# Kernel tuning notes

Measured on AMD Instinct MI355X. Metric: run time of the kernel, lower is better.

Reference implementation:

```python
import jax, jax.numpy as jnp
import numpy as np

TEMPERATURE = 0.5


def _cos_sim_flat(a, b):
    # row-normalize then full similarity matrix, flattened (matches torch.mm(a_n, b_n.T).flatten())
    a_n = a / jnp.linalg.norm(a, axis=1, keepdims=True)
    b_n = b / jnp.linalg.norm(b, axis=1, keepdims=True)
    return (a_n @ b_n.T).reshape(-1)


def setup_inputs() -> dict:
    key = jax.random.key(0)
    k1, k2, k3 = jax.random.split(key, 3)
    N, D = 4096, 2048
    return {
        "x_source": jax.random.normal(k1, (N, D), dtype=jnp.float32),
        "x_bc_target": jax.random.normal(k2, (N, D), dtype=jnp.float32),
        "x_raw_target": jax.random.normal(k3, (N, D), dtype=jnp.float32),
    }


def reference(x_source, x_bc_target, x_raw_target):
    sim_pos = _cos_sim_flat(x_source, x_bc_target)  # [N*N]
    sim_neg = _cos_sim_flat(x_source, x_raw_target)  # [N*N]
    # denom = sum_j exp(sim_neg_j / T); loss_i = -log(exp(sim_pos_i/T)/denom)
    # = -sim_pos_i/T + logsumexp(sim_neg/T); mean over i. Same math as the
    # original scalar loops, computed as one fused reduction.
    log_denom = jax.nn.logsumexp(sim_neg / TEMPERATURE)
    cl_loss = jnp.mean(log_denom - sim_pos / TEMPERATURE)
    return cl_loss
```

## Files before the change

kernel.cpp:

```cpp
#include <hip/hip_runtime.h>
#include <hip/hip_bf16.h>

#define NR 4096
#define DD 2048
#define INV_T 2.0f
#define QSCALE 32.0f
#define ACC_TO_LOGIT (INV_T / (QSCALE * QSCALE))

typedef __attribute__((ext_vector_type(2))) float floatx2;
typedef __attribute__((ext_vector_type(4))) float floatx4;
typedef __attribute__((ext_vector_type(4))) int int4v;
typedef __attribute__((ext_vector_type(8))) int int8v;

static __device__ __forceinline__ void async_copy16(const void* g, void* lds) {
  __builtin_amdgcn_global_load_lds((const __attribute__((address_space(1))) void*)g,
                                   (__attribute__((address_space(3))) void*)lds,
                                   16, 0, 0);
}

__global__ __launch_bounds__(256) void normalize_kernel(
    const float* __restrict__ src, const float* __restrict__ bc,
    const float* __restrict__ raw,
    unsigned char* __restrict__ a8, unsigned char* __restrict__ b8,
    unsigned char* __restrict__ c8, float* __restrict__ zbuf) {
  const int row = blockIdx.x;
  const int mat = blockIdx.y;
  const int tid = threadIdx.x;
  const float* base = (mat == 0) ? src : ((mat == 1) ? bc : raw);
  const float4* b4 = (const float4*)(base + (size_t)row * DD);

  if (mat == 1 && row < 17) {
    const int idx = row * 256 + tid;
    if (idx < 2 * DD + 1) zbuf[idx] = 0.f;
  }

  float4 v0 = b4[tid * 2];
  float4 v1 = b4[tid * 2 + 1];
  float ss = v0.x * v0.x + v0.y * v0.y + v0.z * v0.z + v0.w * v0.w +
             v1.x * v1.x + v1.y * v1.y + v1.z * v1.z + v1.w * v1.w;
  #pragma unroll
  for (int off = 32; off > 0; off >>= 1) ss += __shfl_down(ss, off, 64);

  __shared__ float sred[4];
  __shared__ float sinv;
  if ((tid & 63) == 0) sred[tid >> 6] = ss;
  __syncthreads();
  if (tid == 0) sinv = rsqrtf(sred[0] + sred[1] + sred[2] + sred[3]);
  __syncthreads();
  const float s = sinv * QSCALE;

  int d0 = __builtin_amdgcn_cvt_pk_fp8_f32(v0.x * s, v0.y * s, 0, false);
  d0 = __builtin_amdgcn_cvt_pk_fp8_f32(v0.z * s, v0.w * s, d0, true);
  int d1 = __builtin_amdgcn_cvt_pk_fp8_f32(v1.x * s, v1.y * s, 0, false);
  d1 = __builtin_amdgcn_cvt_pk_fp8_f32(v1.z * s, v1.w * s, d1, true);
  int2 o; o.x = d0; o.y = d1;
  unsigned char* dst =
      ((mat == 0) ? a8 : ((mat == 1) ? b8 : c8)) + (size_t)row * DD + tid * 8;
  *(int2*)dst = o;
}

__global__ __launch_bounds__(256, 2) void gemm_expsum_kernel(
    const unsigned char* __restrict__ a8, const unsigned char* __restrict__ c8,
    float* __restrict__ S_part) {
  __shared__ unsigned char As[2][128 * 128];
  __shared__ unsigned char Cs[2][128 * 128];
  const int tid = threadIdx.x;
  const int lane = tid & 63;
  const int wave = tid >> 6;
  const int wr = wave >> 1;
  const int wc = wave & 1;
  const int quad = lane >> 4;
  const int l16 = lane & 15;
  const int br = blockIdx.x, bc = blockIdx.y;

  floatx4 acc[4][4] = {};

  const int wrow = lane >> 3;
  const int csrc = (lane & 7) ^ (wrow & 7);
  const unsigned char* gA[4];
  const unsigned char* gC[4];
  int ldsOff[4];
  #pragma unroll
  for (int q = 0; q < 4; q++) {
    const int m = wave * 4 + q;
    const int row = m * 8 + wrow;
    gA[q] = a8 + (size_t)(br * 128 + row) * DD + csrc * 16;
    gC[q] = c8 + (size_t)(bc * 128 + row) * DD + csrc * 16;
    ldsOff[q] = m * 1024;
  }

  #pragma unroll
  for (int q = 0; q < 4; q++) {
    async_copy16(gA[q], &As[0][ldsOff[q]]);
    async_copy16(gC[q], &Cs[0][ldsOff[q]]);
    gA[q] += 128; gC[q] += 128;
  }

  #pragma unroll 2
  for (int kt = 0; kt < DD / 128; kt++) {
    const int b = kt & 1;
    __syncthreads();

    if (kt < DD / 128 - 1) {
      #pragma unroll
      for (int q = 0; q < 4; q++) {
        async_copy16(gA[q], &As[b ^ 1][ldsOff[q]]);
        async_copy16(gC[q], &Cs[b ^ 1][ldsOff[q]]);
        gA[q] += 128; gC[q] += 128;
      }
    }

    int8v af[4], bf[4];
    #pragma unroll
    for (int i = 0; i < 4; i++) {
      const int r = wr * 64 + i * 16 + l16;
      const int c0 = (2 * quad) ^ (r & 7);
      const int c1 = (2 * quad + 1) ^ (r & 7);
      int4v lo = *(const int4v*)&As[b][r * 128 + c0 * 16];
      int4v hi = *(const int4v*)&As[b][r * 128 + c1 * 16];
      af[i] = int8v{lo[0], lo[1], lo[2], lo[3], hi[0], hi[1], hi[2], hi[3]};
    }
    #pragma unroll
    for (int j = 0; j < 4; j++) {
      const int r = wc * 64 + j * 16 + l16;
      const int c0 = (2 * quad) ^ (r & 7);
      const int c1 = (2 * quad + 1) ^ (r & 7);
      int4v lo = *(const int4v*)&Cs[b][r * 128 + c0 * 16];
      int4v hi = *(const int4v*)&Cs[b][r * 128 + c1 * 16];
      bf[j] = int8v{lo[0], lo[1], lo[2], lo[3], hi[0], hi[1], hi[2], hi[3]};
    }
    #pragma unroll
    for (int i = 0; i < 4; i++)
      #pragma unroll
      for (int j = 0; j < 4; j++)
        acc[i][j] = __builtin_amdgcn_mfma_scale_f32_16x16x128_f8f6f4(
            af[i], bf[j], acc[i][j], 0 , 0 ,
            0, 0x7F7F7F7F, 0, 0x7F7F7F7F );
  }

  float local = 0.f;
  #pragma unroll
  for (int i = 0; i < 4; i++)
    #pragma unroll
    for (int j = 0; j < 4; j++)
      #pragma unroll
      for (int r = 0; r < 4; r++)
        local += __expf(acc[i][j][r] * ACC_TO_LOGIT);
  #pragma unroll
  for (int off = 32; off > 0; off >>= 1) local += __shfl_down(local, off, 64);
  __shared__ float red[4];
  if (lane == 0) red[wave] = local;
  __syncthreads();
  if (tid == 0) S_part[br * 32 + bc] = red[0] + red[1] + red[2] + red[3];
}

__global__ __launch_bounds__(256) void colsum_finalize_kernel(
    const unsigned char* __restrict__ a8, const unsigned char* __restrict__ b8,
    float* __restrict__ s_a, float* __restrict__ s_b,
    float* __restrict__ counter, const float* __restrict__ S_part,
    float* __restrict__ out) {
  __shared__ float lds[32 * 264];
  const int tid = threadIdx.x;
  const int rt = tid >> 3;
  const int ct = tid & 7;
  const int cg = blockIdx.x & 7;
  const int rg = blockIdx.x >> 3;
  const int cbase = cg * 256 + ct * 32;
  const int rbase = rg * 256 + rt;

  float accA[32], accB[32];
  #pragma unroll
  for (int i = 0; i < 32; i++) { accA[i] = 0.f; accB[i] = 0.f; }

  #pragma unroll
  for (int k = 0; k < 8; k++) {
    const size_t off = (size_t)(rbase + k * 32) * DD + cbase;
    const int8v ra = *(const int8v*)(a8 + off);
    const int8v rb = *(const int8v*)(b8 + off);
    #pragma unroll
    for (int u = 0; u < 8; u++) {
      floatx2 lo = __builtin_amdgcn_cvt_pk_f32_fp8(ra[u], false);
      floatx2 hi = __builtin_amdgcn_cvt_pk_f32_fp8(ra[u], true);
      accA[u * 4 + 0] += lo[0]; accA[u * 4 + 1] += lo[1];
      accA[u * 4 + 2] += hi[0]; accA[u * 4 + 3] += hi[1];
      lo = __builtin_amdgcn_cvt_pk_f32_fp8(rb[u], false);
      hi = __builtin_amdgcn_cvt_pk_f32_fp8(rb[u], true);
      accB[u * 4 + 0] += lo[0]; accB[u * 4 + 1] += lo[1];
      accB[u * 4 + 2] += hi[0]; accB[u * 4 + 3] += hi[1];
    }
  }

  #pragma unroll
  for (int i = 0; i < 32; i += 4)
    *(floatx4*)&lds[rt * 264 + ct * 32 + i] =
        floatx4{accA[i], accA[i + 1], accA[i + 2], accA[i + 3]};
  __syncthreads();
  float sA = 0.f;
  #pragma unroll 8
  for (int r = 0; r < 32; r++) sA += lds[r * 264 + tid];
  atomicAdd(&s_a[cg * 256 + tid], sA);
  __syncthreads();

  #pragma unroll
  for (int i = 0; i < 32; i += 4)
    *(floatx4*)&lds[rt * 264 + ct * 32 + i] =
        floatx4{accB[i], accB[i + 1], accB[i + 2], accB[i + 3]};
  __syncthreads();
  float sB = 0.f;
  #pragma unroll 8
  for (int r = 0; r < 32; r++) sB += lds[r * 264 + tid];
  atomicAdd(&s_b[cg * 256 + tid], sB);

  __threadfence();
  __syncthreads();
  __shared__ bool amLast;
  if (tid == 0) amLast = (atomicAdd(counter, 1.0f) == 127.0f);
  __syncthreads();
  if (!amLast) return;
  __threadfence();

  float dot = 0.f;
  for (int d = tid; d < DD; d += 256)
    dot += atomicAdd(&s_a[d], 0.f) * atomicAdd(&s_b[d], 0.f);
  float se = 0.f;
  for (int i = tid; i < 1024; i += 256) se += S_part[i];

  #pragma unroll
  for (int off = 32; off > 0; off >>= 1) {
    dot += __shfl_down(dot, off, 64);
    se += __shfl_down(se, off, 64);
  }
  __shared__ float redd[4], reds[4];
  if ((tid & 63) == 0) { redd[tid >> 6] = dot; reds[tid >> 6] = se; }
  __syncthreads();
  if (tid == 0) {
    const float dt = redd[0] + redd[1] + redd[2] + redd[3];
    const float st = reds[0] + reds[1] + reds[2] + reds[3];
    out[0] = logf(st) - dt * (ACC_TO_LOGIT / ((float)NR * (float)NR));
  }
}

extern "C" void kernel_launch(void* const* d_in, const int* in_sizes, int n_in,
                              void* d_out, int out_size, void* d_ws, size_t ws_size,
                              hipStream_t stream) {
  const float* src = (const float*)d_in[0];
  const float* bc  = (const float*)d_in[1];
  const float* raw = (const float*)d_in[2];

  char* ws = (char*)d_ws;
  unsigned char* a8 = (unsigned char*)ws;
  unsigned char* b8 = (unsigned char*)(ws + (size_t)8 * 1024 * 1024);
  unsigned char* c8 = (unsigned char*)(ws + (size_t)16 * 1024 * 1024);
  float* zbuf  = (float*)(ws + (size_t)24 * 1024 * 1024);
  float* s_a   = zbuf;
  float* s_b   = zbuf + DD;
  float* counter = zbuf + 2 * DD;
  float* S_part = (float*)(ws + (size_t)24 * 1024 * 1024 + 20480);

  normalize_kernel<<<dim3(NR, 3), 256, 0, stream>>>(src, bc, raw, a8, b8, c8, zbuf);
  gemm_expsum_kernel<<<dim3(32, 32), 256, 0, stream>>>(a8, c8, S_part);
  colsum_finalize_kernel<<<128, 256, 0, stream>>>(a8, b8, s_a, s_b, counter,
                                                  S_part, (float*)d_out);
}
```

Baseline: 178.4 us.

## Pre-pack A operand in MFMA fragment layout and load it directly into registers

The normalize kernel now also writes the source matrix in an MFMA-fragment-ordered layout (A2), so the GEMM loads A fragments straight from global memory into registers with double buffering. The A shared-memory tile and its async copies are removed, and the grid index mapping is swapped so that neighbouring blocks share the same C tile. This cuts LDS traffic and LDS footprint, which may allow higher occupancy. The cost is an extra 8 MB write in normalize, more register pressure from the prefetched A fragments, and direct global loads whose latency must be hidden.

```diff
diff --git a/kernel.cpp b/kernel.cpp
--- a/kernel.cpp
+++ b/kernel.cpp
@@ -21,8 +21,9 @@
 __global__ __launch_bounds__(256) void normalize_kernel(
     const float* __restrict__ src, const float* __restrict__ bc,
     const float* __restrict__ raw,
-    unsigned char* __restrict__ a8, unsigned char* __restrict__ b8,
-    unsigned char* __restrict__ c8, float* __restrict__ zbuf) {
+    unsigned char* __restrict__ a8row, unsigned char* __restrict__ A2,
+    unsigned char* __restrict__ b8, unsigned char* __restrict__ c8,
+    float* __restrict__ zbuf) {
   const int row = blockIdx.x;
   const int mat = blockIdx.y;
   const int tid = threadIdx.x;
@@ -54,15 +55,23 @@
   int d1 = __builtin_amdgcn_cvt_pk_fp8_f32(v1.x * s, v1.y * s, 0, false);
   d1 = __builtin_amdgcn_cvt_pk_fp8_f32(v1.z * s, v1.w * s, d1, true);
   int2 o; o.x = d0; o.y = d1;
-  unsigned char* dst =
-      ((mat == 0) ? a8 : ((mat == 1) ? b8 : c8)) + (size_t)row * DD + tid * 8;
-  *(int2*)dst = o;
+
+  if (mat == 0) {
+    *(int2*)(a8row + (size_t)row * DD + tid * 8) = o;
+    const int kt = tid >> 4, quad = (tid >> 2) & 3;
+    unsigned char* p = A2 +
+        (((size_t)(row >> 4) * 64 + kt * 4 + quad) * 16 + (row & 15)) * 32 +
+        (tid & 3) * 8;
+    *(int2*)p = o;
+  } else {
+    unsigned char* dst = ((mat == 1) ? b8 : c8) + (size_t)row * DD + tid * 8;
+    *(int2*)dst = o;
+  }
 }
 
 __global__ __launch_bounds__(256, 2) void gemm_expsum_kernel(
-    const unsigned char* __restrict__ a8, const unsigned char* __restrict__ c8,
+    const unsigned char* __restrict__ A2, const unsigned char* __restrict__ c8,
     float* __restrict__ S_part) {
-  __shared__ unsigned char As[2][128 * 128];
   __shared__ unsigned char Cs[2][128 * 128];
   const int tid = threadIdx.x;
   const int lane = tid & 63;
@@ -71,71 +80,78 @@
   const int wc = wave & 1;
   const int quad = lane >> 4;
   const int l16 = lane & 15;
-  const int br = blockIdx.x, bc = blockIdx.y;
+  const int bc = blockIdx.x, br = blockIdx.y;
 
   floatx4 acc[4][4] = {};
 
   const int wrow = lane >> 3;
   const int csrc = (lane & 7) ^ (wrow & 7);
-  const unsigned char* gA[4];
   const unsigned char* gC[4];
   int ldsOff[4];
   #pragma unroll
   for (int q = 0; q < 4; q++) {
     const int m = wave * 4 + q;
-    const int row = m * 8 + wrow;
-    gA[q] = a8 + (size_t)(br * 128 + row) * DD + csrc * 16;
-    gC[q] = c8 + (size_t)(bc * 128 + row) * DD + csrc * 16;
+    gC[q] = c8 + (size_t)(bc * 128 + m * 8 + wrow) * DD + csrc * 16;
     ldsOff[q] = m * 1024;
   }
 
+  const unsigned char* pA =
+      A2 + (size_t)(br * 8 + wr * 4) * 32768 + quad * 512 + l16 * 32;
+
+  int4v aLo[2][4], aHi[2][4];
+
   #pragma unroll
   for (int q = 0; q < 4; q++) {
-    async_copy16(gA[q], &As[0][ldsOff[q]]);
     async_copy16(gC[q], &Cs[0][ldsOff[q]]);
-    gA[q] += 128; gC[q] += 128;
+    gC[q] += 128;
+  }
+  #pragma unroll
+  for (int i = 0; i < 4; i++) {
+    const unsigned char* p = pA + (size_t)i * 32768;
+    aLo[0][i] = *(const int4v*)p;
+    aHi[0][i] = *(const int4v*)(p + 16);
   }
 
   #pragma unroll 2
   for (int kt = 0; kt < DD / 128; kt++) {
-    const int b = kt & 1;
+    const int cur = kt & 1;
     __syncthreads();
 
     if (kt < DD / 128 - 1) {
       #pragma unroll
       for (int q = 0; q < 4; q++) {
-        async_copy16(gA[q], &As[b ^ 1][ldsOff[q]]);
-        async_copy16(gC[q], &Cs[b ^ 1][ldsOff[q]]);
-        gA[q] += 128; gC[q] += 128;
+        async_copy16(gC[q], &Cs[cur ^ 1][ldsOff[q]]);
+        gC[q] += 128;
       }
-    }
-
-    int8v af[4], bf[4];
-    #pragma unroll
-    for (int i = 0; i < 4; i++) {
-      const int r = wr * 64 + i * 16 + l16;
-      const int c0 = (2 * quad) ^ (r & 7);
-      const int c1 = (2 * quad + 1) ^ (r & 7);
-      int4v lo = *(const int4v*)&As[b][r * 128 + c0 * 16];
-      int4v hi = *(const int4v*)&As[b][r * 128 + c1 * 16];
-      af[i] = int8v{lo[0], lo[1], lo[2], lo[3], hi[0], hi[1], hi[2], hi[3]};
-    }
+      #pragma unroll
+      for (int i = 0; i < 4; i++) {
+        const unsigned char* p = pA + (size_t)i * 32768 + (kt + 1) * 2048;
+        aLo[cur ^ 1][i] = *(const int4v*)p;
+        aHi[cur ^ 1][i] = *(const int4v*)(p + 16);
+      }
+    }
+
+    int8v bf[4];
     #pragma unroll
     for (int j = 0; j < 4; j++) {
       const int r = wc * 64 + j * 16 + l16;
       const int c0 = (2 * quad) ^ (r & 7);
       const int c1 = (2 * quad + 1) ^ (r & 7);
-      int4v lo = *(const int4v*)&Cs[b][r * 128 + c0 * 16];
-      int4v hi = *(const int4v*)&Cs[b][r * 128 + c1 * 16];
+      int4v lo = *(const int4v*)&Cs[cur][r * 128 + c0 * 16];
+      int4v hi = *(const int4v*)&Cs[cur][r * 128 + c1 * 16];
       bf[j] = int8v{lo[0], lo[1], lo[2], lo[3], hi[0], hi[1], hi[2], hi[3]};
     }
     #pragma unroll
-    for (int i = 0; i < 4; i++)
+    for (int i = 0; i < 4; i++) {
+      const int8v af = int8v{aLo[cur][i][0], aLo[cur][i][1], aLo[cur][i][2],
+                             aLo[cur][i][3], aHi[cur][i][0], aHi[cur][i][1],
+                             aHi[cur][i][2], aHi[cur][i][3]};
       #pragma unroll
       for (int j = 0; j < 4; j++)
         acc[i][j] = __builtin_amdgcn_mfma_scale_f32_16x16x128_f8f6f4(
-            af[i], bf[j], acc[i][j], 0 , 0 ,
+            af, bf[j], acc[i][j], 0 , 0 ,
             0, 0x7F7F7F7F, 0, 0x7F7F7F7F );
+    }
   }
 
   float local = 0.f;
@@ -248,17 +264,19 @@
   const float* raw = (const float*)d_in[2];
 
   char* ws = (char*)d_ws;
-  unsigned char* a8 = (unsigned char*)ws;
-  unsigned char* b8 = (unsigned char*)(ws + (size_t)8 * 1024 * 1024);
-  unsigned char* c8 = (unsigned char*)(ws + (size_t)16 * 1024 * 1024);
-  float* zbuf  = (float*)(ws + (size_t)24 * 1024 * 1024);
+  unsigned char* a8row = (unsigned char*)ws;
+  unsigned char* b8  = (unsigned char*)(ws + (size_t)8 * 1024 * 1024);
+  unsigned char* c8  = (unsigned char*)(ws + (size_t)16 * 1024 * 1024);
+  unsigned char* A2  = (unsigned char*)(ws + (size_t)24 * 1024 * 1024);
+  float* zbuf  = (float*)(ws + (size_t)32 * 1024 * 1024);
   float* s_a   = zbuf;
   float* s_b   = zbuf + DD;
   float* counter = zbuf + 2 * DD;
-  float* S_part = (float*)(ws + (size_t)24 * 1024 * 1024 + 20480);
-
-  normalize_kernel<<<dim3(NR, 3), 256, 0, stream>>>(src, bc, raw, a8, b8, c8, zbuf);
-  gemm_expsum_kernel<<<dim3(32, 32), 256, 0, stream>>>(a8, c8, S_part);
-  colsum_finalize_kernel<<<128, 256, 0, stream>>>(a8, b8, s_a, s_b, counter,
+  float* S_part = (float*)(ws + (size_t)32 * 1024 * 1024 + 20480);
+
+  normalize_kernel<<<dim3(NR, 3), 256, 0, stream>>>(src, bc, raw, a8row, A2,
+                                                    b8, c8, zbuf);
+  gemm_expsum_kernel<<<dim3(32, 32), 256, 0, stream>>>(A2, c8, S_part);
+  colsum_finalize_kernel<<<128, 256, 0, stream>>>(a8row, b8, s_a, s_b, counter,
                                                   S_part, (float*)d_out);
 }
```

Result: no change. 181.6 us (+1.8%).

## Quantize negative-similarity GEMM operands to FP4 and use FP4 MFMA

Applied to the files above, without the earlier changes.

The normalize kernel now also emits an FP4 (e2m1) encoding of the source and raw-target rows, scaled by 64, using a threshold-based encoder. The exp-sum GEMM reads these FP4 operands, halving the bytes loaded per K step and halving the number of K iterations, and runs the scaled MFMA in FP4 mode with the upper operand half zero-padded. The FP8 path stays in place for the positive-term column sums. This reduces memory traffic and MFMA work at the cost of much coarser quantization of the logsumexp term, plus extra encode work in normalization. The block index mapping is also swapped.

```diff
diff --git a/kernel.cpp b/kernel.cpp
--- a/kernel.cpp
+++ b/kernel.cpp
@@ -6,6 +6,8 @@
 #define INV_T 2.0f
 #define QSCALE 32.0f
 #define ACC_TO_LOGIT (INV_T / (QSCALE * QSCALE))
+#define QS4 64.0f
+#define ACC4_TO_LOGIT (INV_T / (QS4 * QS4))
 
 typedef __attribute__((ext_vector_type(2))) float floatx2;
 typedef __attribute__((ext_vector_type(4))) float floatx4;
@@ -18,11 +20,27 @@
                                    16, 0, 0);
 }
 
+static __device__ __forceinline__ unsigned int enc4(float x) {
+  float u = fminf(fabsf(x), 6.0f);
+  int c = (u >= 0.25f) + (u >= 0.75f) + (u >= 1.25f) + (u >= 1.75f) +
+          (u >= 2.5f) + (u >= 3.5f) + (u >= 5.0f);
+  return (unsigned)(c | (x < 0.f ? 8 : 0));
+}
+
+static __device__ __forceinline__ unsigned int pack8_fp4(
+    const float4& v0, const float4& v1, float s) {
+  return enc4(v0.x * s)        | (enc4(v0.y * s) << 4)  |
+         (enc4(v0.z * s) << 8) | (enc4(v0.w * s) << 12) |
+         (enc4(v1.x * s) << 16)| (enc4(v1.y * s) << 20) |
+         (enc4(v1.z * s) << 24)| (enc4(v1.w * s) << 28);
+}
+
 __global__ __launch_bounds__(256) void normalize_kernel(
     const float* __restrict__ src, const float* __restrict__ bc,
     const float* __restrict__ raw,
-    unsigned char* __restrict__ a8, unsigned char* __restrict__ b8,
-    unsigned char* __restrict__ c8, float* __restrict__ zbuf) {
+    unsigned char* __restrict__ a8row, unsigned int* __restrict__ a4,
+    unsigned char* __restrict__ b8, unsigned int* __restrict__ c4,
+    float* __restrict__ zbuf) {
   const int row = blockIdx.x;
   const int mat = blockIdx.y;
   const int tid = threadIdx.x;
@@ -47,20 +65,28 @@
   __syncthreads();
   if (tid == 0) sinv = rsqrtf(sred[0] + sred[1] + sred[2] + sred[3]);
   __syncthreads();
+
+  if (mat == 2) {
+    c4[row * (DD / 8) + tid] = pack8_fp4(v0, v1, sinv * QS4);
+    return;
+  }
+
   const float s = sinv * QSCALE;
-
   int d0 = __builtin_amdgcn_cvt_pk_fp8_f32(v0.x * s, v0.y * s, 0, false);
   d0 = __builtin_amdgcn_cvt_pk_fp8_f32(v0.z * s, v0.w * s, d0, true);
   int d1 = __builtin_amdgcn_cvt_pk_fp8_f32(v1.x * s, v1.y * s, 0, false);
   d1 = __builtin_amdgcn_cvt_pk_fp8_f32(v1.z * s, v1.w * s, d1, true);
   int2 o; o.x = d0; o.y = d1;
-  unsigned char* dst =
-      ((mat == 0) ? a8 : ((mat == 1) ? b8 : c8)) + (size_t)row * DD + tid * 8;
-  *(int2*)dst = o;
+  if (mat == 0) {
+    *(int2*)(a8row + (size_t)row * DD + tid * 8) = o;
+    a4[row * (DD / 8) + tid] = pack8_fp4(v0, v1, sinv * QS4);
+  } else {
+    *(int2*)(b8 + (size_t)row * DD + tid * 8) = o;
+  }
 }
 
 __global__ __launch_bounds__(256, 2) void gemm_expsum_kernel(
-    const unsigned char* __restrict__ a8, const unsigned char* __restrict__ c8,
+    const unsigned char* __restrict__ a4, const unsigned char* __restrict__ c4,
     float* __restrict__ S_part) {
   __shared__ unsigned char As[2][128 * 128];
   __shared__ unsigned char Cs[2][128 * 128];
@@ -71,7 +97,7 @@
   const int wc = wave & 1;
   const int quad = lane >> 4;
   const int l16 = lane & 15;
-  const int br = blockIdx.x, bc = blockIdx.y;
+  const int bc = blockIdx.x, br = blockIdx.y;
 
   floatx4 acc[4][4] = {};
 
@@ -84,8 +110,8 @@
   for (int q = 0; q < 4; q++) {
     const int m = wave * 4 + q;
     const int row = m * 8 + wrow;
-    gA[q] = a8 + (size_t)(br * 128 + row) * DD + csrc * 16;
-    gC[q] = c8 + (size_t)(bc * 128 + row) * DD + csrc * 16;
+    gA[q] = a4 + (size_t)(br * 128 + row) * 1024 + csrc * 16;
+    gC[q] = c4 + (size_t)(bc * 128 + row) * 1024 + csrc * 16;
     ldsOff[q] = m * 1024;
   }
 
@@ -96,46 +122,52 @@
     gA[q] += 128; gC[q] += 128;
   }
 
+  const int NKT = DD / 256;
   #pragma unroll 2
-  for (int kt = 0; kt < DD / 128; kt++) {
-    const int b = kt & 1;
+  for (int kt = 0; kt < NKT; kt++) {
+    const int cur = kt & 1;
     __syncthreads();
 
-    if (kt < DD / 128 - 1) {
+    if (kt < NKT - 1) {
       #pragma unroll
       for (int q = 0; q < 4; q++) {
-        async_copy16(gA[q], &As[b ^ 1][ldsOff[q]]);
-        async_copy16(gC[q], &Cs[b ^ 1][ldsOff[q]]);
+        async_copy16(gA[q], &As[cur ^ 1][ldsOff[q]]);
+        async_copy16(gC[q], &Cs[cur ^ 1][ldsOff[q]]);
         gA[q] += 128; gC[q] += 128;
       }
     }
 
-    int8v af[4], bf[4];
-    #pragma unroll
-    for (int i = 0; i < 4; i++) {
-      const int r = wr * 64 + i * 16 + l16;
-      const int c0 = (2 * quad) ^ (r & 7);
-      const int c1 = (2 * quad + 1) ^ (r & 7);
-      int4v lo = *(const int4v*)&As[b][r * 128 + c0 * 16];
-      int4v hi = *(const int4v*)&As[b][r * 128 + c1 * 16];
-      af[i] = int8v{lo[0], lo[1], lo[2], lo[3], hi[0], hi[1], hi[2], hi[3]};
+    int4v af[2][4], bf[2][4];
+    #pragma unroll
+    for (int s = 0; s < 2; s++) {
+      #pragma unroll
+      for (int i = 0; i < 4; i++) {
+        const int r = wr * 64 + i * 16 + l16;
+        const int pc = (s * 4 + quad) ^ (r & 7);
+        af[s][i] = *(const int4v*)&As[cur][r * 128 + pc * 16];
+      }
+      #pragma unroll
+      for (int j = 0; j < 4; j++) {
+        const int r = wc * 64 + j * 16 + l16;
+        const int pc = (s * 4 + quad) ^ (r & 7);
+        bf[s][j] = *(const int4v*)&Cs[cur][r * 128 + pc * 16];
+      }
     }
     #pragma unroll
-    for (int j = 0; j < 4; j++) {
-      const int r = wc * 64 + j * 16 + l16;
-      const int c0 = (2 * quad) ^ (r & 7);
-      const int c1 = (2 * quad + 1) ^ (r & 7);
-      int4v lo = *(const int4v*)&Cs[b][r * 128 + c0 * 16];
-      int4v hi = *(const int4v*)&Cs[b][r * 128 + c1 * 16];
-      bf[j] = int8v{lo[0], lo[1], lo[2], lo[3], hi[0], hi[1], hi[2], hi[3]};
-    }
-    #pragma unroll
-    for (int i = 0; i < 4; i++)
-      #pragma unroll
-      for (int j = 0; j < 4; j++)
-        acc[i][j] = __builtin_amdgcn_mfma_scale_f32_16x16x128_f8f6f4(
-            af[i], bf[j], acc[i][j], 0 , 0 ,
-            0, 0x7F7F7F7F, 0, 0x7F7F7F7F );
+    for (int s = 0; s < 2; s++)
+      #pragma unroll
+      for (int i = 0; i < 4; i++) {
+        const int8v a8v = int8v{af[s][i][0], af[s][i][1], af[s][i][2],
+                                af[s][i][3], 0, 0, 0, 0};
+        #pragma unroll
+        for (int j = 0; j < 4; j++) {
+          const int8v b8v = int8v{bf[s][j][0], bf[s][j][1], bf[s][j][2],
+                                  bf[s][j][3], 0, 0, 0, 0};
+          acc[i][j] = __builtin_amdgcn_mfma_scale_f32_16x16x128_f8f6f4(
+              a8v, b8v, acc[i][j], 4 , 4 ,
+              0, 0x7F7F7F7F, 0, 0x7F7F7F7F );
+        }
+      }
   }
 
   float local = 0.f;
@@ -145,7 +177,7 @@
     for (int j = 0; j < 4; j++)
       #pragma unroll
       for (int r = 0; r < 4; r++)
-        local += __expf(acc[i][j][r] * ACC_TO_LOGIT);
+        local += __expf(acc[i][j][r] * ACC4_TO_LOGIT);
   #pragma unroll
   for (int off = 32; off > 0; off >>= 1) local += __shfl_down(local, off, 64);
   __shared__ float red[4];
@@ -248,17 +280,20 @@
   const float* raw = (const float*)d_in[2];
 
   char* ws = (char*)d_ws;
-  unsigned char* a8 = (unsigned char*)ws;
+  unsigned char* a8row = (unsigned char*)ws;
   unsigned char* b8 = (unsigned char*)(ws + (size_t)8 * 1024 * 1024);
-  unsigned char* c8 = (unsigned char*)(ws + (size_t)16 * 1024 * 1024);
+  unsigned int* a4  = (unsigned int*)(ws + (size_t)16 * 1024 * 1024);
+  unsigned int* c4  = (unsigned int*)(ws + (size_t)20 * 1024 * 1024);
   float* zbuf  = (float*)(ws + (size_t)24 * 1024 * 1024);
   float* s_a   = zbuf;
   float* s_b   = zbuf + DD;
   float* counter = zbuf + 2 * DD;
   float* S_part = (float*)(ws + (size_t)24 * 1024 * 1024 + 20480);
 
-  normalize_kernel<<<dim3(NR, 3), 256, 0, stream>>>(src, bc, raw, a8, b8, c8, zbuf);
-  gemm_expsum_kernel<<<dim3(32, 32), 256, 0, stream>>>(a8, c8, S_part);
-  colsum_finalize_kernel<<<128, 256, 0, stream>>>(a8, b8, s_a, s_b, counter,
+  normalize_kernel<<<dim3(NR, 3), 256, 0, stream>>>(src, bc, raw, a8row, a4,
+                                                    b8, c4, zbuf);
+  gemm_expsum_kernel<<<dim3(32, 32), 256, 0, stream>>>(
+      (const unsigned char*)a4, (const unsigned char*)c4, S_part);
+  colsum_finalize_kernel<<<128, 256, 0, stream>>>(a8row, b8, s_a, s_b, counter,
                                                   S_part, (float*)d_out);
 }
```

Result: faster. 166.1 us, median of 2 (-6.9%).
